# Optimization experiments

Measured on AMD Instinct MI355X. Metric: run time of the kernel, lower is better.

## Reference

```python
import jax, jax.numpy as jnp
import numpy as np

B, S, DM, H = 2, 2048, 1024, 16
D = DM // H
SCALE = D ** -0.5


def setup_inputs() -> dict:
    key = jax.random.key(0)
    k1, k2, k3 = jax.random.split(key, 3)
    x = jax.random.normal(k1, (B, S, DM), dtype=jnp.float32)
    w_qkv = jax.random.normal(k2, (DM, 3 * DM), dtype=jnp.float32) * (DM ** -0.5)
    b_qkv = jnp.zeros((3 * DM,), dtype=jnp.float32)
    w_out = jax.random.normal(k3, (DM, DM), dtype=jnp.float32) * (DM ** -0.5)
    b_out = jnp.zeros((DM,), dtype=jnp.float32)
    return {"x": x, "w_qkv": w_qkv, "b_qkv": b_qkv, "w_out": w_out, "b_out": b_out}


def reference(x, w_qkv, b_qkv, w_out, b_out):
    b, n, _ = x.shape
    qkv = x @ w_qkv + b_qkv                          # [b, n, 3*dm]
    q, k, v = jnp.split(qkv, 3, axis=-1)
    # b n (h d) -> b h n d
    split = lambda t: t.reshape(b, n, H, D).transpose(0, 2, 1, 3)
    q, k, v = split(q), split(k), split(v)
    dots = jnp.einsum('bhid,bhjd->bhij', q, k) * SCALE
    # causal (fore) mask: -inf above the diagonal
    causal = jnp.tril(jnp.ones((n, n), dtype=bool))
    dots = jnp.where(causal, dots, -jnp.inf)
    attn = jax.nn.softmax(dots, axis=-1)
    out = jnp.einsum('bhij,bhjd->bhid', attn, v)     # [b, h, n, d]
    out = out.transpose(0, 2, 1, 3).reshape(b, n, H * D)
    return out @ w_out + b_out
```

## Files before the change

### kernel.cpp

```cpp
#include <hip/hip_runtime.h>
#include <hip/hip_bf16.h>

#define NB 2
#define NS 2048
#define NDM 1024
#define NH 16
#define ND 64
#define NM (NB * NS)
#define RS 3072
#define C1 0.1803368801111243f
#define THR_RAW 44.36141956f

typedef __attribute__((ext_vector_type(8))) short bf16x8;
typedef __attribute__((ext_vector_type(4))) float f32x4;

__device__ __forceinline__ unsigned short f2bf(float f) {
    unsigned int u = __float_as_uint(f);
    u += 0x7fffu + ((u >> 16) & 1u);
    return (unsigned short)(u >> 16);
}

__device__ __forceinline__ void gload16(const unsigned short* g, unsigned short* l) {
    __builtin_amdgcn_global_load_lds(
        (const __attribute__((address_space(1))) void*)g,
        (__attribute__((address_space(3))) void*)l, 16, 0, 0);
}

__global__ __launch_bounds__(256)
void convert_bf16(const float* __restrict__ in, unsigned short* __restrict__ out, int n8) {
    int i = blockIdx.x * 256 + threadIdx.x;
    const int stride = gridDim.x * 256;
    for (; i < n8; i += stride) {
        const float4 a = ((const float4*)in)[i * 2];
        const float4 b = ((const float4*)in)[i * 2 + 1];
        bf16x8 v;
        v[0] = (short)f2bf(a.x); v[1] = (short)f2bf(a.y);
        v[2] = (short)f2bf(a.z); v[3] = (short)f2bf(a.w);
        v[4] = (short)f2bf(b.x); v[5] = (short)f2bf(b.y);
        v[6] = (short)f2bf(b.z); v[7] = (short)f2bf(b.w);
        *(bf16x8*)(out + (size_t)i * 8) = v;
    }
}

__global__ __launch_bounds__(256)
void transpose_bf16(const float* __restrict__ W, unsigned short* __restrict__ WT,
                    int K, int N) {
    __shared__ float Ts[64][65];
    const int n0 = blockIdx.x * 64, k0 = blockIdx.y * 64;
    const int t = threadIdx.x;
    {
        const int c4 = (t & 15) * 4;
        #pragma unroll
        for (int p = 0; p < 4; p++) {
            const int r = (t >> 4) + p * 16;
            const float4 v = *(const float4*)(W + (size_t)(k0 + r) * N + n0 + c4);
            Ts[r][c4] = v.x; Ts[r][c4 + 1] = v.y; Ts[r][c4 + 2] = v.z; Ts[r][c4 + 3] = v.w;
        }
    }
    __syncthreads();
    {
        const int cc8 = (t & 7) * 8;
        #pragma unroll
        for (int p = 0; p < 2; p++) {
            const int rr = (t >> 3) + p * 32;
            bf16x8 v;
            #pragma unroll
            for (int j = 0; j < 8; j++) v[j] = (short)f2bf(Ts[cc8 + j][rr]);
            *(bf16x8*)(WT + (size_t)(n0 + rr) * K + k0 + cc8) = v;
        }
    }
}

__global__ __launch_bounds__(256)
void vtrans(const unsigned short* __restrict__ qkvb, unsigned short* __restrict__ vT) {
    __shared__ unsigned short Ts[64][65];
    const int st = blockIdx.x, bh = blockIdx.y;
    const int h = bh & (NH - 1), b = bh >> 4;
    const int t = threadIdx.x;
    {
        const int c8 = (t & 7) * 8;
        #pragma unroll
        for (int p = 0; p < 2; p++) {
            const int r = (t >> 3) + p * 32;
            const unsigned short* src =
                qkvb + (size_t)(b * NS + st * 64 + r) * RS + 2 * NDM + h * ND + c8;
            const bf16x8 v = *(const bf16x8*)src;
            #pragma unroll
            for (int j = 0; j < 8; j++) Ts[r][c8 + j] = (unsigned short)v[j];
        }
    }
    __syncthreads();
    {
        #pragma unroll
        for (int i = 0; i < 2; i++) {
            const int u = t + i * 256;
            const int d = u >> 3, cg = (u & 7) * 8;
            bf16x8 v;
            #pragma unroll
            for (int j = 0; j < 8; j++) v[j] = (short)Ts[cg + j][d];
            *(bf16x8*)(vT + ((size_t)bh * ND + d) * NS + st * 64 + cg) = v;
        }
    }
}

template<int MODE>
__global__ __launch_bounds__(256)
void gemm128(const unsigned short* __restrict__ A, const unsigned short* __restrict__ BT,
             const float* __restrict__ bias, void* __restrict__ Cv,
             int M, int N, int K) {
    __shared__ unsigned short As[2][128 * 32];
    __shared__ unsigned short Bs[2][128 * 32];

    const int t = threadIdx.x, lane = t & 63, wv = t >> 6;
    const int wm = wv >> 1, wn = wv & 1;
    const int m0 = blockIdx.y * 128, n0 = blockIdx.x * 128;
    const int fr = lane & 15, fg = lane >> 4;

    f32x4 acc[4][4];
    #pragma unroll
    for (int m = 0; m < 4; m++)
        #pragma unroll
        for (int n = 0; n < 4; n++)
            #pragma unroll
            for (int r = 0; r < 4; r++) acc[m][n][r] = 0.f;

#define GSTAGE(buf, kk)                                                               \
    {                                                                                 \
        _Pragma("unroll")                                                             \
        for (int i = 0; i < 2; i++) {                                                 \
            const int u = t + i * 256;                                                \
            const int row = u >> 2;                                                   \
            const int grp = (u & 3) ^ ((row ^ (row >> 2)) & 3);                       \
            gload16(A  + (size_t)(m0 + row) * K + (kk) + grp * 8,                     \
                    &As[buf][(i * 256 + wv * 64) * 8]);                               \
            gload16(BT + (size_t)(n0 + row) * K + (kk) + grp * 8,                     \
                    &Bs[buf][(i * 256 + wv * 64) * 8]);                               \
        }                                                                             \
    }

#define GCOMPUTE(buf)                                                                 \
    {                                                                                 \
        bf16x8 af[4], bfv[4];                                                         \
        _Pragma("unroll")                                                             \
        for (int m = 0; m < 4; m++) {                                                 \
            const int row = wm * 64 + m * 16 + fr;                                    \
            af[m] = *(const bf16x8*)&As[buf][row * 32 +                               \
                        ((fg ^ ((row ^ (row >> 2)) & 3)) << 3)];                      \
        }                                                                             \
        _Pragma("unroll")                                                             \
        for (int n = 0; n < 4; n++) {                                                 \
            const int row = wn * 64 + n * 16 + fr;                                    \
            bfv[n] = *(const bf16x8*)&Bs[buf][row * 32 +                              \
                        ((fg ^ ((row ^ (row >> 2)) & 3)) << 3)];                      \
        }                                                                             \
        __builtin_amdgcn_s_setprio(1);                                                \
        _Pragma("unroll")                                                             \
        for (int m = 0; m < 4; m++)                                                   \
            _Pragma("unroll")                                                         \
            for (int n = 0; n < 4; n++)                                               \
                acc[m][n] = __builtin_amdgcn_mfma_f32_16x16x32_bf16(                  \
                    af[m], bfv[n], acc[m][n], 0, 0, 0);                               \
        __builtin_amdgcn_s_setprio(0);                                                \
    }

    GSTAGE(0, 0);
    for (int k0 = 0; k0 < K; k0 += 64) {
        __syncthreads();
        GSTAGE(1, k0 + 32);
        GCOMPUTE(0);
        __syncthreads();
        if (k0 + 64 < K) GSTAGE(0, k0 + 64);
        GCOMPUTE(1);
    }
#undef GSTAGE
#undef GCOMPUTE

    #pragma unroll
    for (int m = 0; m < 4; m++)
        #pragma unroll
        for (int n = 0; n < 4; n++) {
            const int col = n0 + wn * 64 + n * 16 + fr;
            const float bb = bias[col];
            #pragma unroll
            for (int rg = 0; rg < 4; rg++) {
                const int row = m0 + wm * 64 + m * 16 + fg * 4 + rg;
                const float v = acc[m][n][rg] + bb;
                if (MODE == 0) ((float*)Cv)[(size_t)row * N + col] = v;
                else ((unsigned short*)Cv)[(size_t)row * N + col] = f2bf(v);
            }
        }
}

__global__ __launch_bounds__(256)
void gemm128x64(const unsigned short* __restrict__ A, const unsigned short* __restrict__ BT,
                const float* __restrict__ bias, float* __restrict__ C,
                int M, int N, int K) {
    __shared__ unsigned short As[2][128 * 32];
    __shared__ unsigned short Bs[2][64 * 32];

    const int t = threadIdx.x, lane = t & 63, wv = t >> 6;
    const int wm = wv >> 1, wn = wv & 1;
    const int m0 = blockIdx.y * 128, n0 = blockIdx.x * 64;
    const int fr = lane & 15, fg = lane >> 4;

    f32x4 acc[4][2];
    #pragma unroll
    for (int m = 0; m < 4; m++)
        #pragma unroll
        for (int n = 0; n < 2; n++)
            #pragma unroll
            for (int r = 0; r < 4; r++) acc[m][n][r] = 0.f;

#define G2STAGE(buf, kk)                                                              \
    {                                                                                 \
        _Pragma("unroll")                                                             \
        for (int i = 0; i < 2; i++) {                                                 \
            const int u = t + i * 256;                                                \
            const int row = u >> 2;                                                   \
            const int grp = (u & 3) ^ ((row ^ (row >> 2)) & 3);                       \
            gload16(A + (size_t)(m0 + row) * K + (kk) + grp * 8,                      \
                    &As[buf][(i * 256 + wv * 64) * 8]);                               \
        }                                                                             \
        {                                                                             \
            const int row = t >> 2;                                                   \
            const int grp = (t & 3) ^ ((row ^ (row >> 2)) & 3);                       \
            gload16(BT + (size_t)(n0 + row) * K + (kk) + grp * 8,                     \
                    &Bs[buf][(wv * 64) * 8]);                                         \
        }                                                                             \
    }

#define G2COMPUTE(buf)                                                                \
    {                                                                                 \
        bf16x8 af[4], bfv[2];                                                         \
        _Pragma("unroll")                                                             \
        for (int m = 0; m < 4; m++) {                                                 \
            const int row = wm * 64 + m * 16 + fr;                                    \
            af[m] = *(const bf16x8*)&As[buf][row * 32 +                               \
                        ((fg ^ ((row ^ (row >> 2)) & 3)) << 3)];                      \
        }                                                                             \
        _Pragma("unroll")                                                             \
        for (int n = 0; n < 2; n++) {                                                 \
            const int row = wn * 32 + n * 16 + fr;                                    \
            bfv[n] = *(const bf16x8*)&Bs[buf][row * 32 +                              \
                        ((fg ^ ((row ^ (row >> 2)) & 3)) << 3)];                      \
        }                                                                             \
        __builtin_amdgcn_s_setprio(1);                                                \
        _Pragma("unroll")                                                             \
        for (int m = 0; m < 4; m++)                                                   \
            _Pragma("unroll")                                                         \
            for (int n = 0; n < 2; n++)                                               \
                acc[m][n] = __builtin_amdgcn_mfma_f32_16x16x32_bf16(                  \
                    af[m], bfv[n], acc[m][n], 0, 0, 0);                               \
        __builtin_amdgcn_s_setprio(0);                                                \
    }

    G2STAGE(0, 0);
    for (int k0 = 0; k0 < K; k0 += 64) {
        __syncthreads();
        G2STAGE(1, k0 + 32);
        G2COMPUTE(0);
        __syncthreads();
        if (k0 + 64 < K) G2STAGE(0, k0 + 64);
        G2COMPUTE(1);
    }
#undef G2STAGE
#undef G2COMPUTE

    #pragma unroll
    for (int m = 0; m < 4; m++)
        #pragma unroll
        for (int n = 0; n < 2; n++) {
            const int col = n0 + wn * 32 + n * 16 + fr;
            const float bb = bias[col];
            #pragma unroll
            for (int rg = 0; rg < 4; rg++) {
                const int row = m0 + wm * 64 + m * 16 + fg * 4 + rg;
                C[(size_t)row * N + col] = acc[m][n][rg] + bb;
            }
        }
}

__global__ __launch_bounds__(256)
void attn_mfma(const unsigned short* __restrict__ qkvb, const unsigned short* __restrict__ vT,
               unsigned short* __restrict__ atto) {
    const int bx = blockIdx.x;
    const int qt = (NS / 64 - 1) - (bx >> 5);
    const int bh = bx & 31;
    const int h = bh & (NH - 1), b = bh >> 4;
    const int q0 = qt * 64;
    const int t = threadIdx.x, lane = t & 63, wv = t >> 6;
    const int fr = lane & 15, fg = lane >> 4;

    __shared__ unsigned short Kt[2][128 * 64];
    __shared__ unsigned short Vt[2][64 * 128];
    __shared__ unsigned short Ps[4][16 * 128];

    const unsigned short* kb = qkvb + (size_t)b * NS * RS + NDM + h * ND;
    const unsigned short* vb = vT + (size_t)bh * ND * NS;

    bf16x8 qf[2];
    {
        const unsigned short* qrow =
            qkvb + (size_t)(b * NS + q0 + wv * 16 + fr) * RS + h * ND;
        qf[0] = *(const bf16x8*)(qrow + fg * 8);
        qf[1] = *(const bf16x8*)(qrow + 32 + fg * 8);
    }

    f32x4 oacc[4];
    #pragma unroll
    for (int d = 0; d < 4; d++)
        #pragma unroll
        for (int r = 0; r < 4; r++) oacc[d][r] = 0.f;
    float mrow = -INFINITY;
    float nmC  = INFINITY;
    float lrow = 0.f;

    const int ntiles = (qt >> 1) + 1;

#define STAGE_KV(cbuf, jtile)                                                        \
    {                                                                                \
        _Pragma("unroll")                                                            \
        for (int i = 0; i < 4; i++) {                                                \
            const int u = t + i * 256;                                               \
            const int row = u >> 3;                                                  \
            const int grp = (u & 7) ^ (row & 7);                                     \
            gload16(kb + (size_t)((jtile) * 128 + row) * RS + grp * 8,               \
                    &Kt[cbuf][(i * 256 + wv * 64) * 8]);                             \
        }                                                                            \
        _Pragma("unroll")                                                            \
        for (int i = 0; i < 4; i++) {                                                \
            const int u = t + i * 256;                                               \
            const int row = u >> 4;                                                  \
            const int grp = (u & 15) ^ (row & 7);                                    \
            gload16(vb + (size_t)row * NS + (jtile) * 128 + grp * 8,                 \
                    &Vt[cbuf][(i * 256 + wv * 64) * 8]);                             \
        }                                                                            \
    }

    STAGE_KV(0, 0);

    for (int jt = 0; jt < ntiles; jt++) {
        const int cur = jt & 1;
        __syncthreads();
        if (jt + 1 < ntiles) STAGE_KV(cur ^ 1, jt + 1);
        const unsigned short* Ktc = Kt[cur];
        const unsigned short* Vtc = Vt[cur];

        f32x4 sacc[8];
        __builtin_amdgcn_s_setprio(1);
        #pragma unroll
        for (int kbi = 0; kbi < 8; kbi++) {
            #pragma unroll
            for (int r = 0; r < 4; r++) sacc[kbi][r] = 0.f;
            const int row = kbi * 16 + fr;
            const bf16x8 kf0 = *(const bf16x8*)&Ktc[row * 64 + (((fg) ^ (row & 7)) << 3)];
            const bf16x8 kf1 = *(const bf16x8*)&Ktc[row * 64 + (((4 + fg) ^ (row & 7)) << 3)];
            sacc[kbi] = __builtin_amdgcn_mfma_f32_16x16x32_bf16(kf0, qf[0], sacc[kbi], 0, 0, 0);
            sacc[kbi] = __builtin_amdgcn_mfma_f32_16x16x32_bf16(kf1, qf[1], sacc[kbi], 0, 0, 0);
        }
        __builtin_amdgcn_s_setprio(0);

        if (jt == ntiles - 1) {
            const int qg = q0 + wv * 16 + fr;
            #pragma unroll
            for (int kbi = 0; kbi < 8; kbi++) {
                #pragma unroll
                for (int reg = 0; reg < 4; reg++) {
                    const int keyg = jt * 128 + kbi * 16 + fg * 4 + reg;
                    if (keyg > qg) sacc[kbi][reg] = -INFINITY;
                }
            }
        }

        float mk[8];
        #pragma unroll
        for (int kbi = 0; kbi < 8; kbi++)
            mk[kbi] = fmaxf(fmaxf(sacc[kbi][0], sacc[kbi][1]),
                            fmaxf(sacc[kbi][2], sacc[kbi][3]));
        float pm = fmaxf(fmaxf(fmaxf(mk[0], mk[1]), fmaxf(mk[2], mk[3])),
                         fmaxf(fmaxf(mk[4], mk[5]), fmaxf(mk[6], mk[7])));
        pm = fmaxf(pm, __shfl_xor(pm, 16));
        pm = fmaxf(pm, __shfl_xor(pm, 32));

        if (__any(pm > mrow + THR_RAW)) {
            const float mn = fmaxf(mrow, pm);
            const float alpha = __builtin_amdgcn_exp2f((mrow - mn) * C1);
            mrow = mn;
            nmC = -mn * C1;
            lrow *= alpha;
            #pragma unroll
            for (int reg = 0; reg < 4; reg++) {
                const float aq = __shfl(alpha, fg * 4 + reg);
                #pragma unroll
                for (int dblk = 0; dblk < 4; dblk++) oacc[dblk][reg] *= aq;
            }
        }

        float psum = 0.f;
        #pragma unroll
        for (int kbi = 0; kbi < 8; kbi++) {
            #pragma unroll
            for (int reg = 0; reg < 4; reg++) {
                const float p = __builtin_amdgcn_exp2f(fmaf(sacc[kbi][reg], C1, nmC));
                sacc[kbi][reg] = p;
                psum += p;
            }
        }
        psum += __shfl_xor(psum, 16);
        psum += __shfl_xor(psum, 32);
        lrow += psum;

        #pragma unroll
        for (int kbi = 0; kbi < 8; kbi++) {
            unsigned int w0, w1;
            asm("v_cvt_pk_bf16_f32 %0, %1, %2"
                : "=v"(w0) : "v"(sacc[kbi][0]), "v"(sacc[kbi][1]));
            asm("v_cvt_pk_bf16_f32 %0, %1, %2"
                : "=v"(w1) : "v"(sacc[kbi][2]), "v"(sacc[kbi][3]));
            const int grp = (kbi * 2 + (fg >> 1)) ^ (fr & 7);
            const int base = fr * 128 + grp * 8 + (fg & 1) * 4;
            *(unsigned int*)&Ps[wv][base]     = w0;
            *(unsigned int*)&Ps[wv][base + 2] = w1;
        }

        bf16x8 pf[4];
        #pragma unroll
        for (int ks = 0; ks < 4; ks++)
            pf[ks] = *(const bf16x8*)&Ps[wv][fr * 128 + (((ks * 4 + fg) ^ (fr & 7)) << 3)];
        __builtin_amdgcn_s_setprio(1);
        #pragma unroll
        for (int dblk = 0; dblk < 4; dblk++) {
            const int vrow = dblk * 16 + fr;
            #pragma unroll
            for (int ks = 0; ks < 4; ks++) {
                const bf16x8 vf =
                    *(const bf16x8*)&Vtc[vrow * 128 + (((ks * 4 + fg) ^ (vrow & 7)) << 3)];
                oacc[dblk] = __builtin_amdgcn_mfma_f32_16x16x32_bf16(
                    pf[ks], vf, oacc[dblk], 0, 0, 0);
            }
        }
        __builtin_amdgcn_s_setprio(0);
    }
#undef STAGE_KV

    const float rl = 1.f / lrow;
    #pragma unroll
    for (int reg = 0; reg < 4; reg++) {
        const float inv = __shfl(rl, fg * 4 + reg);
        const int row = q0 + wv * 16 + fg * 4 + reg;
        unsigned short* dst = atto + ((size_t)b * NS + row) * NDM + h * ND;
        #pragma unroll
        for (int dblk = 0; dblk < 4; dblk++)
            dst[dblk * 16 + fr] = f2bf(oacc[dblk][reg] * inv);
    }
}

extern "C" void kernel_launch(void* const* d_in, const int* in_sizes, int n_in,
                              void* d_out, int out_size, void* d_ws, size_t ws_size,
                              hipStream_t stream) {
    const float* x     = (const float*)d_in[0];
    const float* w_qkv = (const float*)d_in[1];
    const float* b_qkv = (const float*)d_in[2];
    const float* w_out = (const float*)d_in[3];
    const float* b_out = (const float*)d_in[4];
    float* out = (float*)d_out;

    unsigned short* xb   = (unsigned short*)d_ws;
    unsigned short* wqT  = xb   + (size_t)NM * NDM;
    unsigned short* woT  = wqT  + (size_t)3 * NDM * NDM;
    unsigned short* qkvb = woT  + (size_t)NDM * NDM;
    unsigned short* vT   = qkvb + (size_t)NM * 3 * NDM;
    unsigned short* atto = xb;

    convert_bf16<<<2048, 256, 0, stream>>>(x, xb, NM * NDM / 8);
    transpose_bf16<<<dim3(3 * NDM / 64, NDM / 64), 256, 0, stream>>>(w_qkv, wqT, NDM, 3 * NDM);
    transpose_bf16<<<dim3(NDM / 64, NDM / 64), 256, 0, stream>>>(w_out, woT, NDM, NDM);

    gemm128<1><<<dim3(3 * NDM / 128, NM / 128), 256, 0, stream>>>(
        xb, wqT, b_qkv, qkvb, NM, 3 * NDM, NDM);

    vtrans<<<dim3(NS / 64, NB * NH), 256, 0, stream>>>(qkvb, vT);

    attn_mfma<<<dim3((NS / 64) * NB * NH), 256, 0, stream>>>(qkvb, vT, atto);

    gemm128x64<<<dim3(NDM / 64, NM / 128), 256, 0, stream>>>(
        atto, woT, b_out, out, NM, NDM, NDM);
}
```

Measured before the change: 185.2 us.

## Switch attention to 32x32x16 MFMA with register-resident P and larger query tiles

Rewrites the attention kernel to use 32x32x16 bf16 MFMA. Each wave now owns 32 query rows, so a block covers 128 queries, and K/V tiles shrink to 64 keys. The softmax probabilities are repacked in registers with a cross-half lane shuffle instead of going through shared memory. Per-row max and sum now need only one shuffle, and the output is written with packed bf16 stores. The intent is to cut LDS traffic and shuffle overhead and raise MFMA efficiency; in exchange it launches half as many blocks and adds more masked tiles on the diagonal.

```diff
diff --git a/kernel.cpp b/kernel.cpp
--- a/kernel.cpp
+++ b/kernel.cpp
@@ -13,6 +13,7 @@
 
 typedef __attribute__((ext_vector_type(8))) short bf16x8;
 typedef __attribute__((ext_vector_type(4))) float f32x4;
+typedef __attribute__((ext_vector_type(16))) float f32x16;
 
 __device__ __forceinline__ unsigned short f2bf(float f) {
     unsigned int u = __float_as_uint(f);
@@ -284,55 +285,57 @@
 void attn_mfma(const unsigned short* __restrict__ qkvb, const unsigned short* __restrict__ vT,
                unsigned short* __restrict__ atto) {
     const int bx = blockIdx.x;
-    const int qt = (NS / 64 - 1) - (bx >> 5);
+    const int qt = (NS / 128 - 1) - (bx >> 5);
     const int bh = bx & 31;
     const int h = bh & (NH - 1), b = bh >> 4;
-    const int q0 = qt * 64;
+    const int q0 = qt * 128;
     const int t = threadIdx.x, lane = t & 63, wv = t >> 6;
-    const int fr = lane & 15, fg = lane >> 4;
-
-    __shared__ unsigned short Kt[2][128 * 64];
-    __shared__ unsigned short Vt[2][64 * 128];
-    __shared__ unsigned short Ps[4][16 * 128];
+    const int l31 = lane & 31, hf = lane >> 5;
+    const bool hb = hf != 0;
+
+    __shared__ unsigned short Kt[2][64 * 64];
+    __shared__ unsigned short Vt[2][64 * 64];
 
     const unsigned short* kb = qkvb + (size_t)b * NS * RS + NDM + h * ND;
     const unsigned short* vb = vT + (size_t)bh * ND * NS;
 
-    bf16x8 qf[2];
+    bf16x8 qf[4];
     {
         const unsigned short* qrow =
-            qkvb + (size_t)(b * NS + q0 + wv * 16 + fr) * RS + h * ND;
-        qf[0] = *(const bf16x8*)(qrow + fg * 8);
-        qf[1] = *(const bf16x8*)(qrow + 32 + fg * 8);
-    }
-
-    f32x4 oacc[4];
+            qkvb + (size_t)(b * NS + q0 + wv * 32 + l31) * RS + h * ND + hf * 8;
+        qf[0] = *(const bf16x8*)(qrow);
+        qf[1] = *(const bf16x8*)(qrow + 16);
+        qf[2] = *(const bf16x8*)(qrow + 32);
+        qf[3] = *(const bf16x8*)(qrow + 48);
+    }
+
+    f32x16 oacc[2];
     #pragma unroll
-    for (int d = 0; d < 4; d++)
-        #pragma unroll
-        for (int r = 0; r < 4; r++) oacc[d][r] = 0.f;
+    for (int d2 = 0; d2 < 2; d2++)
+        #pragma unroll
+        for (int r = 0; r < 16; r++) oacc[d2][r] = 0.f;
     float mrow = -INFINITY;
     float nmC  = INFINITY;
     float lrow = 0.f;
 
-    const int ntiles = (qt >> 1) + 1;
+    const int ntiles = 2 * qt + 2;
 
 #define STAGE_KV(cbuf, jtile)                                                        \
     {                                                                                \
         _Pragma("unroll")                                                            \
-        for (int i = 0; i < 4; i++) {                                                \
+        for (int i = 0; i < 2; i++) {                                                \
             const int u = t + i * 256;                                               \
             const int row = u >> 3;                                                  \
-            const int grp = (u & 7) ^ (row & 7);                                     \
-            gload16(kb + (size_t)((jtile) * 128 + row) * RS + grp * 8,               \
+            const int gs = (u & 7) ^ (row & 7);                                      \
+            gload16(kb + (size_t)((jtile) * 64 + row) * RS + gs * 8,                 \
                     &Kt[cbuf][(i * 256 + wv * 64) * 8]);                             \
         }                                                                            \
         _Pragma("unroll")                                                            \
-        for (int i = 0; i < 4; i++) {                                                \
+        for (int i = 0; i < 2; i++) {                                                \
             const int u = t + i * 256;                                               \
-            const int row = u >> 4;                                                  \
-            const int grp = (u & 15) ^ (row & 7);                                    \
-            gload16(vb + (size_t)row * NS + (jtile) * 128 + grp * 8,                 \
+            const int row = u >> 3;                                                  \
+            const int gs = (u & 7) ^ (row & 7);                                      \
+            gload16(vb + (size_t)row * NS + (jtile) * 64 + gs * 8,                   \
                     &Vt[cbuf][(i * 256 + wv * 64) * 8]);                             \
         }                                                                            \
     }
@@ -346,40 +349,41 @@
         const unsigned short* Ktc = Kt[cur];
         const unsigned short* Vtc = Vt[cur];
 
-        f32x4 sacc[8];
+        f32x16 sacc[2];
+        #pragma unroll
+        for (int kb2 = 0; kb2 < 2; kb2++)
+            #pragma unroll
+            for (int r = 0; r < 16; r++) sacc[kb2][r] = 0.f;
         __builtin_amdgcn_s_setprio(1);
         #pragma unroll
-        for (int kbi = 0; kbi < 8; kbi++) {
-            #pragma unroll
-            for (int r = 0; r < 4; r++) sacc[kbi][r] = 0.f;
-            const int row = kbi * 16 + fr;
-            const bf16x8 kf0 = *(const bf16x8*)&Ktc[row * 64 + (((fg) ^ (row & 7)) << 3)];
-            const bf16x8 kf1 = *(const bf16x8*)&Ktc[row * 64 + (((4 + fg) ^ (row & 7)) << 3)];
-            sacc[kbi] = __builtin_amdgcn_mfma_f32_16x16x32_bf16(kf0, qf[0], sacc[kbi], 0, 0, 0);
-            sacc[kbi] = __builtin_amdgcn_mfma_f32_16x16x32_bf16(kf1, qf[1], sacc[kbi], 0, 0, 0);
+        for (int kb2 = 0; kb2 < 2; kb2++) {
+            const int row = kb2 * 32 + l31;
+            #pragma unroll
+            for (int kd = 0; kd < 4; kd++) {
+                const int s = (2 * kd + hf) ^ (row & 7);
+                const bf16x8 kf = *(const bf16x8*)&Ktc[row * 64 + s * 8];
+                sacc[kb2] = __builtin_amdgcn_mfma_f32_32x32x16_bf16(
+                    kf, qf[kd], sacc[kb2], 0, 0, 0);
+            }
         }
         __builtin_amdgcn_s_setprio(0);
 
-        if (jt == ntiles - 1) {
-            const int qg = q0 + wv * 16 + fr;
-            #pragma unroll
-            for (int kbi = 0; kbi < 8; kbi++) {
+        if (jt >= ntiles - 2) {
+            const int qg = q0 + wv * 32 + l31;
+            #pragma unroll
+            for (int kb2 = 0; kb2 < 2; kb2++)
                 #pragma unroll
-                for (int reg = 0; reg < 4; reg++) {
-                    const int keyg = jt * 128 + kbi * 16 + fg * 4 + reg;
-                    if (keyg > qg) sacc[kbi][reg] = -INFINITY;
+                for (int r = 0; r < 16; r++) {
+                    const int key = jt * 64 + kb2 * 32 + (r & 3) + 8 * (r >> 2) + 4 * hf;
+                    if (key > qg) sacc[kb2][r] = -INFINITY;
                 }
-            }
-        }
-
-        float mk[8];
-        #pragma unroll
-        for (int kbi = 0; kbi < 8; kbi++)
-            mk[kbi] = fmaxf(fmaxf(sacc[kbi][0], sacc[kbi][1]),
-                            fmaxf(sacc[kbi][2], sacc[kbi][3]));
-        float pm = fmaxf(fmaxf(fmaxf(mk[0], mk[1]), fmaxf(mk[2], mk[3])),
-                         fmaxf(fmaxf(mk[4], mk[5]), fmaxf(mk[6], mk[7])));
-        pm = fmaxf(pm, __shfl_xor(pm, 16));
+        }
+
+        float pm = sacc[0][0];
+        #pragma unroll
+        for (int r = 1; r < 16; r++) pm = fmaxf(pm, sacc[0][r]);
+        #pragma unroll
+        for (int r = 0; r < 16; r++) pm = fmaxf(pm, sacc[1][r]);
         pm = fmaxf(pm, __shfl_xor(pm, 32));
 
         if (__any(pm > mrow + THR_RAW)) {
@@ -389,70 +393,80 @@
             nmC = -mn * C1;
             lrow *= alpha;
             #pragma unroll
-            for (int reg = 0; reg < 4; reg++) {
-                const float aq = __shfl(alpha, fg * 4 + reg);
+            for (int d2 = 0; d2 < 2; d2++)
                 #pragma unroll
-                for (int dblk = 0; dblk < 4; dblk++) oacc[dblk][reg] *= aq;
-            }
+                for (int r = 0; r < 16; r++) oacc[d2][r] *= alpha;
         }
 
         float psum = 0.f;
         #pragma unroll
-        for (int kbi = 0; kbi < 8; kbi++) {
-            #pragma unroll
-            for (int reg = 0; reg < 4; reg++) {
-                const float p = __builtin_amdgcn_exp2f(fmaf(sacc[kbi][reg], C1, nmC));
-                sacc[kbi][reg] = p;
+        for (int kb2 = 0; kb2 < 2; kb2++)
+            #pragma unroll
+            for (int r = 0; r < 16; r++) {
+                const float p = __builtin_amdgcn_exp2f(fmaf(sacc[kb2][r], C1, nmC));
+                sacc[kb2][r] = p;
                 psum += p;
             }
-        }
-        psum += __shfl_xor(psum, 16);
         psum += __shfl_xor(psum, 32);
         lrow += psum;
 
-        #pragma unroll
-        for (int kbi = 0; kbi < 8; kbi++) {
-            unsigned int w0, w1;
-            asm("v_cvt_pk_bf16_f32 %0, %1, %2"
-                : "=v"(w0) : "v"(sacc[kbi][0]), "v"(sacc[kbi][1]));
-            asm("v_cvt_pk_bf16_f32 %0, %1, %2"
-                : "=v"(w1) : "v"(sacc[kbi][2]), "v"(sacc[kbi][3]));
-            const int grp = (kbi * 2 + (fg >> 1)) ^ (fr & 7);
-            const int base = fr * 128 + grp * 8 + (fg & 1) * 4;
-            *(unsigned int*)&Ps[wv][base]     = w0;
-            *(unsigned int*)&Ps[wv][base + 2] = w1;
-        }
+        unsigned int W[2][4][2];
+        #pragma unroll
+        for (int kb2 = 0; kb2 < 2; kb2++)
+            #pragma unroll
+            for (int r2 = 0; r2 < 4; r2++)
+                #pragma unroll
+                for (int c = 0; c < 2; c++)
+                    asm("v_cvt_pk_bf16_f32 %0, %1, %2" : "=v"(W[kb2][r2][c])
+                        : "v"(sacc[kb2][r2 * 4 + c * 2]), "v"(sacc[kb2][r2 * 4 + c * 2 + 1]));
 
         bf16x8 pf[4];
         #pragma unroll
-        for (int ks = 0; ks < 4; ks++)
-            pf[ks] = *(const bf16x8*)&Ps[wv][fr * 128 + (((ks * 4 + fg) ^ (fr & 7)) << 3)];
+        for (int ks = 0; ks < 4; ks++) {
+            const int kb2 = ks >> 1, s = ks & 1;
+            const unsigned int X0 = hb ? W[kb2][2 * s][0] : W[kb2][2 * s + 1][0];
+            const unsigned int X1 = hb ? W[kb2][2 * s][1] : W[kb2][2 * s + 1][1];
+            const unsigned int Y0 = __shfl_xor(X0, 32);
+            const unsigned int Y1 = __shfl_xor(X1, 32);
+            unsigned int u[4];
+            u[0] = hb ? Y0 : W[kb2][2 * s][0];
+            u[1] = hb ? Y1 : W[kb2][2 * s][1];
+            u[2] = hb ? W[kb2][2 * s + 1][0] : Y0;
+            u[3] = hb ? W[kb2][2 * s + 1][1] : Y1;
+            pf[ks] = *(bf16x8*)u;
+        }
+
         __builtin_amdgcn_s_setprio(1);
         #pragma unroll
-        for (int dblk = 0; dblk < 4; dblk++) {
-            const int vrow = dblk * 16 + fr;
+        for (int d2 = 0; d2 < 2; d2++) {
+            const int row = d2 * 32 + l31;
             #pragma unroll
             for (int ks = 0; ks < 4; ks++) {
-                const bf16x8 vf =
-                    *(const bf16x8*)&Vtc[vrow * 128 + (((ks * 4 + fg) ^ (vrow & 7)) << 3)];
-                oacc[dblk] = __builtin_amdgcn_mfma_f32_16x16x32_bf16(
-                    pf[ks], vf, oacc[dblk], 0, 0, 0);
+                const int s = (2 * ks + hf) ^ (row & 7);
+                const bf16x8 vf = *(const bf16x8*)&Vtc[row * 64 + s * 8];
+                oacc[d2] = __builtin_amdgcn_mfma_f32_32x32x16_bf16(
+                    vf, pf[ks], oacc[d2], 0, 0, 0);
             }
         }
         __builtin_amdgcn_s_setprio(0);
     }
 #undef STAGE_KV
 
-    const float rl = 1.f / lrow;
+    const float inv = 1.f / lrow;
+    const int q = q0 + wv * 32 + l31;
+    unsigned short* dst = atto + ((size_t)b * NS + q) * NDM + h * ND;
     #pragma unroll
-    for (int reg = 0; reg < 4; reg++) {
-        const float inv = __shfl(rl, fg * 4 + reg);
-        const int row = q0 + wv * 16 + fg * 4 + reg;
-        unsigned short* dst = atto + ((size_t)b * NS + row) * NDM + h * ND;
-        #pragma unroll
-        for (int dblk = 0; dblk < 4; dblk++)
-            dst[dblk * 16 + fr] = f2bf(oacc[dblk][reg] * inv);
-    }
+    for (int d2 = 0; d2 < 2; d2++)
+        #pragma unroll
+        for (int r2 = 0; r2 < 4; r2++)
+            #pragma unroll
+            for (int c = 0; c < 2; c++) {
+                unsigned int w;
+                const float a0 = oacc[d2][r2 * 4 + c * 2] * inv;
+                const float a1 = oacc[d2][r2 * 4 + c * 2 + 1] * inv;
+                asm("v_cvt_pk_bf16_f32 %0, %1, %2" : "=v"(w) : "v"(a0), "v"(a1));
+                *(unsigned int*)&dst[d2 * 32 + r2 * 8 + hf * 4 + c * 2] = w;
+            }
 }
 
 extern "C" void kernel_launch(void* const* d_in, const int* in_sizes, int n_in,
@@ -481,7 +495,7 @@
 
     vtrans<<<dim3(NS / 64, NB * NH), 256, 0, stream>>>(qkvb, vT);
 
-    attn_mfma<<<dim3((NS / 64) * NB * NH), 256, 0, stream>>>(qkvb, vT, atto);
+    attn_mfma<<<dim3((NS / 128) * NB * NH), 256, 0, stream>>>(qkvb, vT, atto);
 
     gemm128x64<<<dim3(NDM / 64, NM / 128), 256, 0, stream>>>(
         atto, woT, b_out, out, NM, NDM, NDM);
```

Result: slower. 199.1 us (+7.5%).
